# Optimization experiments

Hardware: AMD Instinct MI355X
Metric: run time of the kernel (lower is better)

## Reference

```python
import jax, jax.numpy as jnp
import numpy as np

N = 100000
E = 1600000
F_IN = 128
F_HID = 128


def gcn_conv(x, src, dst, deg_inv_sqrt, W, b, n_nodes):
    # x: [N, Fin] -> [N, Fout]; symmetric-normalized aggregation with self-loops
    h = x @ W  # [N, Fout]
    norm = deg_inv_sqrt[src] * deg_inv_sqrt[dst]  # [E+N] (self-loops appended)
    msgs = h[src] * norm[:, None]  # [E+N, Fout]
    out = jax.ops.segment_sum(msgs, dst, num_segments=n_nodes)
    return out + b


def setup_inputs() -> dict:
    key = jax.random.key(0)
    k = jax.random.split(key, 8)
    x = jax.random.normal(k[0], (N, F_IN), dtype=jnp.float32)
    edge_index = jax.random.randint(k[1], (2, E), 0, N, dtype=jnp.int32)
    s = 1.0 / np.sqrt(F_IN)
    W1 = jax.random.uniform(k[2], (F_IN, F_HID), jnp.float32, -s, s)
    b1 = jnp.zeros((F_HID,), jnp.float32)
    s2 = 1.0 / np.sqrt(F_HID)
    W2 = jax.random.uniform(k[3], (F_HID, F_HID), jnp.float32, -s2, s2)
    b2 = jnp.zeros((F_HID,), jnp.float32)
    W3 = jax.random.uniform(k[4], (F_HID, 1), jnp.float32, -s2, s2)
    b3 = jnp.zeros((1,), jnp.float32)
    return {"x": x, "edge_index": edge_index, "W1": W1, "b1": b1,
            "W2": W2, "b2": b2, "W3": W3, "b3": b3}


def reference(x, edge_index, W1, b1, W2, b2, W3, b3):
    n = x.shape[0]
    loops = jnp.arange(n, dtype=edge_index.dtype)
    src = jnp.concatenate([edge_index[0], loops])  # add self-loops
    dst = jnp.concatenate([edge_index[1], loops])
    deg = jax.ops.segment_sum(jnp.ones_like(dst, dtype=x.dtype), dst, num_segments=n)
    deg_inv_sqrt = jnp.where(deg > 0, jax.lax.rsqrt(deg), 0.0)

    h = gcn_conv(x, src, dst, deg_inv_sqrt, W1, b1, n)
    h = jax.nn.relu(h)  # dropout is identity at inference
    h = gcn_conv(h, src, dst, deg_inv_sqrt, W2, b2, n)
    h = jax.nn.relu(h)
    h = gcn_conv(h, src, dst, deg_inv_sqrt, W3, b3, n)
    return jax.nn.sigmoid(h)  # [N, 1]
```

## Files before the change

### kernel.cpp

```cpp
#include <hip/hip_runtime.h>
#include <cstdint>
#include <cstddef>

#define NN 100000
#define NE 1600000
#define FD 128
#define NXCD 8
#define RNODES ((NN + NXCD - 1) / NXCD)

typedef int vi4 __attribute__((ext_vector_type(4)));

__device__ __forceinline__ float bf_lo(uint32_t u) { return __uint_as_float(u << 16); }
__device__ __forceinline__ float bf_hi(uint32_t u) { return __uint_as_float(u & 0xffff0000u); }
__device__ __forceinline__ uint32_t bf_pack(float a, float b) {
    uint32_t ua = __float_as_uint(a), ub = __float_as_uint(b);
    ua += 0x7fffu + ((ua >> 16) & 1u);
    ub += 0x7fffu + ((ub >> 16) & 1u);
    return (ua >> 16) | (ub & 0xffff0000u);
}

__global__ __launch_bounds__(256) void k_hist(const int* __restrict__ dst,
                                              int* __restrict__ cnt, int e) {
    const int xcd   = blockIdx.x & 7;
    const int chunk = blockIdx.x >> 3;
    const int lo = xcd * RNODES;
    const int hi = lo + RNODES;
    const int base = chunk * 1024 + threadIdx.x * 4;
    if (base >= e) return;
    vi4 d4 = __builtin_nontemporal_load((const vi4*)(dst + base));
    #pragma unroll
    for (int j = 0; j < 4; ++j) {
        int d = d4[j];
        if (d >= lo && d < hi) atomicAdd(&cnt[d], 1);
    }
}

__global__ __launch_bounds__(1024) void k_scan1(const int* __restrict__ cnt,
                                                int* __restrict__ excl,
                                                int* __restrict__ bsum, int n) {
    __shared__ int sh[1024];
    int i = blockIdx.x * 1024 + threadIdx.x;
    int v = (i < n) ? cnt[i] : 0;
    sh[threadIdx.x] = v;
    __syncthreads();
    for (int off = 1; off < 1024; off <<= 1) {
        int t = (threadIdx.x >= off) ? sh[threadIdx.x - off] : 0;
        __syncthreads();
        sh[threadIdx.x] += t;
        __syncthreads();
    }
    if (i < n) excl[i] = sh[threadIdx.x] - v;
    if (threadIdx.x == 1023) bsum[blockIdx.x] = sh[1023];
}

__global__ void k_scan2(int* __restrict__ bsum, int nb) {
    __shared__ int sh[128];
    int t = threadIdx.x;
    int v = (t < nb) ? bsum[t] : 0;
    sh[t] = v;
    __syncthreads();
    for (int off = 1; off < 128; off <<= 1) {
        int u = (t >= off) ? sh[t - off] : 0;
        __syncthreads();
        sh[t] += u;
        __syncthreads();
    }
    if (t < nb) bsum[t] = sh[t] - v;
}

__global__ void k_scan3(int* __restrict__ excl, const int* __restrict__ bsum,
                        int* __restrict__ cursor, const int* __restrict__ cnt,
                        float* __restrict__ dis, int n, int e) {
    int i = blockIdx.x * blockDim.x + threadIdx.x;
    if (i < n) {
        int v = excl[i] + bsum[i >> 10];
        excl[i] = v;
        cursor[i] = v;
        dis[i] = rsqrtf((float)(cnt[i] + 1));
    }
    if (i == 0) excl[n] = e;
}

__global__ __launch_bounds__(256) void k_fill(const int* __restrict__ src,
                                              const int* __restrict__ dst,
                                              int* __restrict__ cursor,
                                              uint2* __restrict__ colw,
                                              const float* __restrict__ dis, int e) {
    const int xcd   = blockIdx.x & 7;
    const int chunk = blockIdx.x >> 3;
    const int lo = xcd * RNODES;
    const int hi = lo + RNODES;
    const int base = chunk * 1024 + threadIdx.x * 4;
    if (base >= e) return;
    vi4 d4 = __builtin_nontemporal_load((const vi4*)(dst + base));
    vi4 s4 = __builtin_nontemporal_load((const vi4*)(src + base));
    #pragma unroll
    for (int j = 0; j < 4; ++j) {
        int d = d4[j];
        if (d >= lo && d < hi) {
            int s   = s4[j];
            int pos = atomicAdd(&cursor[d], 1);
            uint2 cw;
            cw.x = (uint32_t)s;
            cw.y = __float_as_uint(dis[s] * dis[d]);
            colw[pos] = cw;
        }
    }
}

template <typename TIN>
__global__ __launch_bounds__(256) void k_gemm(const TIN* __restrict__ X,
                                              const float* __restrict__ W,
                                              unsigned short* __restrict__ H, int n) {
    __shared__ float At[64][68];
    __shared__ float Ws[64][64];
    const int t  = threadIdx.x;
    const int tx = t & 15;
    const int ty = t >> 4;
    const int rb = blockIdx.x * 64;
    const int cb = blockIdx.y * 64;

    float acc[4][4] = {};

    for (int c = 0; c < 2; ++c) {
        #pragma unroll
        for (int r = 0; r < 4; ++r) {
            int f   = t + 256 * r;
            int row = f >> 4;
            int kc  = (f & 15) << 2;
            int grow = rb + row;
            float4 v = make_float4(0.f, 0.f, 0.f, 0.f);
            if (grow < n) {
                if constexpr (sizeof(TIN) == 4) {
                    v = *(const float4*)((const float*)X + (size_t)grow * FD + c * 64 + kc);
                } else {
                    uint2 p = *(const uint2*)((const unsigned short*)X + (size_t)grow * FD + c * 64 + kc);
                    v.x = bf_lo(p.x); v.y = bf_hi(p.x);
                    v.z = bf_lo(p.y); v.w = bf_hi(p.y);
                }
            }
            At[kc + 0][row] = v.x;
            At[kc + 1][row] = v.y;
            At[kc + 2][row] = v.z;
            At[kc + 3][row] = v.w;
            *(float4*)&Ws[row][kc] =
                *(const float4*)(W + (size_t)(c * 64 + row) * FD + cb + kc);
        }
        __syncthreads();
        #pragma unroll 8
        for (int k = 0; k < 64; ++k) {
            float4 a = *(const float4*)&At[k][ty * 4];
            float4 b = *(const float4*)&Ws[k][tx * 4];
            acc[0][0] = fmaf(a.x, b.x, acc[0][0]);
            acc[0][1] = fmaf(a.x, b.y, acc[0][1]);
            acc[0][2] = fmaf(a.x, b.z, acc[0][2]);
            acc[0][3] = fmaf(a.x, b.w, acc[0][3]);
            acc[1][0] = fmaf(a.y, b.x, acc[1][0]);
            acc[1][1] = fmaf(a.y, b.y, acc[1][1]);
            acc[1][2] = fmaf(a.y, b.z, acc[1][2]);
            acc[1][3] = fmaf(a.y, b.w, acc[1][3]);
            acc[2][0] = fmaf(a.z, b.x, acc[2][0]);
            acc[2][1] = fmaf(a.z, b.y, acc[2][1]);
            acc[2][2] = fmaf(a.z, b.z, acc[2][2]);
            acc[2][3] = fmaf(a.z, b.w, acc[2][3]);
            acc[3][0] = fmaf(a.w, b.x, acc[3][0]);
            acc[3][1] = fmaf(a.w, b.y, acc[3][1]);
            acc[3][2] = fmaf(a.w, b.z, acc[3][2]);
            acc[3][3] = fmaf(a.w, b.w, acc[3][3]);
        }
        __syncthreads();
    }

    #pragma unroll
    for (int i = 0; i < 4; ++i) {
        int grow = rb + ty * 4 + i;
        if (grow < n) {
            uint2 p;
            p.x = bf_pack(acc[i][0], acc[i][1]);
            p.y = bf_pack(acc[i][2], acc[i][3]);
            *(uint2*)(H + (size_t)grow * FD + cb + tx * 4) = p;
        }
    }
}

template <int MODE>
__global__ __launch_bounds__(256) void k_agg(const unsigned short* __restrict__ h,
                                             const float* __restrict__ dis,
                                             const int* __restrict__ rp,
                                             const uint2* __restrict__ colw,
                                             const float* __restrict__ bias,
                                             const float* __restrict__ W3,
                                             unsigned short* __restrict__ out,
                                             float* __restrict__ outf, int n) {
    const uint32_t* h32 = (const uint32_t*)h;
    int wid  = (int)((blockIdx.x * (size_t)blockDim.x + threadIdx.x) >> 6);
    int lane = threadIdx.x & 63;
    int w2 = __builtin_amdgcn_readfirstlane(wid);
    int i0 = 2 * w2;
    if (i0 >= n) return;
    int i1 = i0 + 1;
    const bool has1 = (i1 < n);

    const int e00 = rp[i0];
    const int e01 = rp[i0 + 1];
    const int e11 = has1 ? rp[i0 + 2] : e01;

    float di0 = dis[i0];
    float di1 = has1 ? dis[i1] : 0.f;
    float2 acc0, acc1;
    {
        uint32_t su0 = h32[(size_t)i0 * 64 + lane];
        float q0 = di0 * di0;
        acc0.x = bf_lo(su0) * q0; acc0.y = bf_hi(su0) * q0;
        if (has1) {
            uint32_t su1 = h32[(size_t)i1 * 64 + lane];
            float q1 = di1 * di1;
            acc1.x = bf_lo(su1) * q1; acc1.y = bf_hi(su1) * q1;
        } else { acc1.x = acc1.y = 0.f; }
    }

    const int ng0 = (e01 - e00 + 15) >> 4;
    const int ng1 = (e11 - e01 + 15) >> 4;
    const int ng  = ng0 > ng1 ? ng0 : ng1;

    for (int g = 0; g < ng; ++g) {
        const bool do0 = (g < ng0), do1 = (g < ng1);
        int s0[16], s1[16];
        float w0_[16], w1_[16];
        uint32_t v0[16], v1[16];
        if (do0) {
            const int jb = e00 + g * 16;
            if (jb + 16 <= e01) {
                #pragma unroll
                for (int q = 0; q < 16; ++q) {
                    uint2 cw = colw[jb + q];
                    s0[q] = (int)cw.x; w0_[q] = __uint_as_float(cw.y);
                }
            } else {
                #pragma unroll
                for (int q = 0; q < 16; ++q) {
                    int idx = jb + q;
                    int c   = idx < e01 ? idx : e01 - 1;
                    uint2 cw = colw[c];
                    s0[q]  = (int)cw.x;
                    w0_[q] = idx < e01 ? __uint_as_float(cw.y) : 0.f;
                }
            }
        }
        if (do1) {
            const int jb = e01 + g * 16;
            if (jb + 16 <= e11) {
                #pragma unroll
                for (int q = 0; q < 16; ++q) {
                    uint2 cw = colw[jb + q];
                    s1[q] = (int)cw.x; w1_[q] = __uint_as_float(cw.y);
                }
            } else {
                #pragma unroll
                for (int q = 0; q < 16; ++q) {
                    int idx = jb + q;
                    int c   = idx < e11 ? idx : e11 - 1;
                    uint2 cw = colw[c];
                    s1[q]  = (int)cw.x;
                    w1_[q] = idx < e11 ? __uint_as_float(cw.y) : 0.f;
                }
            }
        }
        if (do0) {
            #pragma unroll
            for (int q = 0; q < 16; ++q)
                v0[q] = h32[(size_t)s0[q] * 64 + lane];
        }
        if (do1) {
            #pragma unroll
            for (int q = 0; q < 16; ++q)
                v1[q] = h32[(size_t)s1[q] * 64 + lane];
        }
        if (do0) {
            #pragma unroll
            for (int q = 0; q < 16; ++q) {
                acc0.x = fmaf(w0_[q], bf_lo(v0[q]), acc0.x);
                acc0.y = fmaf(w0_[q], bf_hi(v0[q]), acc0.y);
            }
        }
        if (do1) {
            #pragma unroll
            for (int q = 0; q < 16; ++q) {
                acc1.x = fmaf(w1_[q], bf_lo(v1[q]), acc1.x);
                acc1.y = fmaf(w1_[q], bf_hi(v1[q]), acc1.y);
            }
        }
    }

    float2 b = ((const float2*)bias)[lane];
    acc0.x = fmaxf(acc0.x + b.x, 0.f);
    acc0.y = fmaxf(acc0.y + b.y, 0.f);
    acc1.x = fmaxf(acc1.x + b.x, 0.f);
    acc1.y = fmaxf(acc1.y + b.y, 0.f);

    if (MODE == 0) {
        ((uint32_t*)out)[(size_t)i0 * 64 + lane] = bf_pack(acc0.x, acc0.y);
        if (has1)
            ((uint32_t*)out)[(size_t)i1 * 64 + lane] = bf_pack(acc1.x, acc1.y);
    } else {
        float2 w3 = ((const float2*)W3)[lane];
        float d0 = acc0.x * w3.x + acc0.y * w3.y;
        float d1 = acc1.x * w3.x + acc1.y * w3.y;
        #pragma unroll
        for (int off = 32; off; off >>= 1) {
            d0 += __shfl_xor(d0, off);
            d1 += __shfl_xor(d1, off);
        }
        if (lane == 0) {
            outf[i0] = d0;
            if (has1) outf[i1] = d1;
        }
    }
}

__global__ __launch_bounds__(256) void k_agg1(const float* __restrict__ h3,
                                              const float* __restrict__ dis,
                                              const int* __restrict__ rp,
                                              const uint2* __restrict__ colw,
                                              const float* __restrict__ b3,
                                              float* __restrict__ out, int n) {
    int i    = (int)((blockIdx.x * (size_t)blockDim.x + threadIdx.x) >> 6);
    int lane = threadIdx.x & 63;
    if (i >= n) return;
    float di  = dis[i];
    float acc = (lane == 0) ? di * di * h3[i] : 0.f;
    const int e0 = rp[i], e1 = rp[i + 1];
    for (int base = e0 + lane; base < e1; base += 64) {
        uint2 cw = colw[base];
        acc = fmaf(__uint_as_float(cw.y), h3[(int)cw.x], acc);
    }
    #pragma unroll
    for (int off = 32; off; off >>= 1) acc += __shfl_xor(acc, off);
    if (lane == 0) {
        float v = acc + b3[0];
        out[i] = 1.f / (1.f + expf(-v));
    }
}

static inline size_t alg(size_t x) { return (x + 255) & ~(size_t)255; }

extern "C" void kernel_launch(void* const* d_in, const int* in_sizes, int n_in,
                              void* d_out, int out_size, void* d_ws, size_t ws_size,
                              hipStream_t stream) {
    const float* x   = (const float*)d_in[0];
    const int*   ei  = (const int*)d_in[1];
    const float* W1  = (const float*)d_in[2];
    const float* b1  = (const float*)d_in[3];
    const float* W2  = (const float*)d_in[4];
    const float* b2  = (const float*)d_in[5];
    const float* W3  = (const float*)d_in[6];
    const float* b3  = (const float*)d_in[7];
    float*       out = (float*)d_out;

    const int n = NN, e = NE;
    const int* src = ei;
    const int* dst = ei + e;

    char* w = (char*)d_ws;
    float* dis    = (float*)w;  w += alg((size_t)n * 4);
    int*   cnt    = (int*)w;    w += alg((size_t)n * 4);
    int*   rp     = (int*)w;    w += alg((size_t)(n + 1) * 4);
    int*   cursor = (int*)w;    w += alg((size_t)n * 4);
    int*   bsum   = (int*)w;    w += alg((size_t)128 * 4);
    uint2* colw   = (uint2*)w;  w += alg((size_t)e * 8);
    unsigned short* bufA = (unsigned short*)w; w += alg((size_t)n * FD * 2);
    unsigned short* bufB = (unsigned short*)w; w += alg((size_t)n * FD * 2);
    float* h3     = (float*)w;  w += alg((size_t)n * 4);

    hipMemsetAsync(cnt, 0, (size_t)n * 4, stream);

    const int B = 256;
    const int gN = (n + B - 1) / B;
    const int nScan = (n + 1023) / 1024;
    const int nChunk = (e + 1023) / 1024;

    k_hist<<<nChunk * NXCD, B, 0, stream>>>(dst, cnt, e);
    k_scan1<<<nScan, 1024, 0, stream>>>(cnt, rp, bsum, n);
    k_scan2<<<1, 128, 0, stream>>>(bsum, nScan);
    k_scan3<<<gN, B, 0, stream>>>(rp, bsum, cursor, cnt, dis, n, e);
    k_fill<<<nChunk * NXCD, B, 0, stream>>>(src, dst, cursor, colw, dis, e);

    dim3 gGemm((n + 63) / 64, 2);
    const int nWave2  = (n + 1) / 2;
    const int gWave2  = (nWave2 * 64 + B - 1) / B;
    const int gWave   = (n * 64 + B - 1) / B;

    k_gemm<float><<<gGemm, B, 0, stream>>>(x, W1, bufA, n);
    k_agg<0><<<gWave2, B, 0, stream>>>(bufA, dis, rp, colw, b1, W3, bufB, h3, n);
    k_gemm<unsigned short><<<gGemm, B, 0, stream>>>(bufB, W2, bufA, n);
    k_agg<1><<<gWave2, B, 0, stream>>>(bufA, dis, rp, colw, b2, W3, bufB, h3, n);
    k_agg1<<<gWave, B, 0, stream>>>(h3, dis, rp, colw, b3, out, n);
}
```

Before: 531.4 us.

## Pre-partition edges into per-XCD buckets before histogram and CSR fill

```diff
diff --git a/kernel.cpp b/kernel.cpp
--- a/kernel.cpp
+++ b/kernel.cpp
@@ -7,6 +7,7 @@
 #define FD 128
 #define NXCD 8
 #define RNODES ((NN + NXCD - 1) / NXCD)
+#define CAP 208192
 
 typedef int vi4 __attribute__((ext_vector_type(4)));
 
@@ -19,20 +20,53 @@
     return (ua >> 16) | (ub & 0xffff0000u);
 }
 
-__global__ __launch_bounds__(256) void k_hist(const int* __restrict__ dst,
-                                              int* __restrict__ cnt, int e) {
-    const int xcd   = blockIdx.x & 7;
-    const int chunk = blockIdx.x >> 3;
+__global__ __launch_bounds__(256) void k_part(const int* __restrict__ src,
+                                              const int* __restrict__ dst,
+                                              uint32_t* __restrict__ bkt,
+                                              int* __restrict__ bcnt, int e) {
+    __shared__ int scnt[8];
+    __shared__ int sbase[8];
+    if (threadIdx.x < 8) scnt[threadIdx.x] = 0;
+    __syncthreads();
+    const int base = blockIdx.x * 1024 + threadIdx.x * 4;
+    const bool valid = base < e;
+    int b_[4]; int r_[4]; uint32_t u_[4];
+    if (valid) {
+        vi4 d4 = __builtin_nontemporal_load((const vi4*)(dst + base));
+        vi4 s4 = __builtin_nontemporal_load((const vi4*)(src + base));
+        #pragma unroll
+        for (int j = 0; j < 4; ++j) {
+            int d = d4[j], s = s4[j];
+            int b = d / RNODES;
+            b_[j] = b;
+            u_[j] = ((uint32_t)(d - b * RNODES) << 17) | (uint32_t)s;
+            r_[j] = atomicAdd(&scnt[b], 1);
+        }
+    }
+    __syncthreads();
+    if (threadIdx.x < 8)
+        sbase[threadIdx.x] = atomicAdd(&bcnt[threadIdx.x], scnt[threadIdx.x]);
+    __syncthreads();
+    if (valid) {
+        #pragma unroll
+        for (int j = 0; j < 4; ++j) {
+            int b = b_[j];
+            bkt[(size_t)b * CAP + sbase[b] + r_[j]] = u_[j];
+        }
+    }
+}
+
+__global__ __launch_bounds__(256) void k_hist2(const uint32_t* __restrict__ bkt,
+                                               const int* __restrict__ bcnt,
+                                               int* __restrict__ cnt) {
+    const int xcd  = blockIdx.x & 7;
+    const int blk  = blockIdx.x >> 3;
+    const int nblk = (int)(gridDim.x >> 3);
+    const int m = bcnt[xcd];
+    const uint32_t* B = bkt + (size_t)xcd * CAP;
     const int lo = xcd * RNODES;
-    const int hi = lo + RNODES;
-    const int base = chunk * 1024 + threadIdx.x * 4;
-    if (base >= e) return;
-    vi4 d4 = __builtin_nontemporal_load((const vi4*)(dst + base));
-    #pragma unroll
-    for (int j = 0; j < 4; ++j) {
-        int d = d4[j];
-        if (d >= lo && d < hi) atomicAdd(&cnt[d], 1);
-    }
+    for (int i = blk * 256 + threadIdx.x; i < m; i += nblk * 256)
+        atomicAdd(&cnt[lo + (int)(B[i] >> 17)], 1);
 }
 
 __global__ __launch_bounds__(1024) void k_scan1(const int* __restrict__ cnt,
@@ -81,30 +115,26 @@
     if (i == 0) excl[n] = e;
 }
 
-__global__ __launch_bounds__(256) void k_fill(const int* __restrict__ src,
-                                              const int* __restrict__ dst,
-                                              int* __restrict__ cursor,
-                                              uint2* __restrict__ colw,
-                                              const float* __restrict__ dis, int e) {
-    const int xcd   = blockIdx.x & 7;
-    const int chunk = blockIdx.x >> 3;
+__global__ __launch_bounds__(256) void k_fill2(const uint32_t* __restrict__ bkt,
+                                               const int* __restrict__ bcnt,
+                                               int* __restrict__ cursor,
+                                               uint2* __restrict__ colw,
+                                               const float* __restrict__ dis) {
+    const int xcd  = blockIdx.x & 7;
+    const int blk  = blockIdx.x >> 3;
+    const int nblk = (int)(gridDim.x >> 3);
+    const int m = bcnt[xcd];
+    const uint32_t* B = bkt + (size_t)xcd * CAP;
     const int lo = xcd * RNODES;
-    const int hi = lo + RNODES;
-    const int base = chunk * 1024 + threadIdx.x * 4;
-    if (base >= e) return;
-    vi4 d4 = __builtin_nontemporal_load((const vi4*)(dst + base));
-    vi4 s4 = __builtin_nontemporal_load((const vi4*)(src + base));
-    #pragma unroll
-    for (int j = 0; j < 4; ++j) {
-        int d = d4[j];
-        if (d >= lo && d < hi) {
-            int s   = s4[j];
-            int pos = atomicAdd(&cursor[d], 1);
-            uint2 cw;
-            cw.x = (uint32_t)s;
-            cw.y = __float_as_uint(dis[s] * dis[d]);
-            colw[pos] = cw;
-        }
+    for (int i = blk * 256 + threadIdx.x; i < m; i += nblk * 256) {
+        uint32_t u = B[i];
+        int s = (int)(u & 0x1FFFFu);
+        int d = lo + (int)(u >> 17);
+        int pos = atomicAdd(&cursor[d], 1);
+        uint2 cw;
+        cw.x = (uint32_t)s;
+        cw.y = __float_as_uint(dis[s] * dis[d]);
+        colw[pos] = cw;
     }
 }
 
@@ -364,26 +394,30 @@
     char* w = (char*)d_ws;
     float* dis    = (float*)w;  w += alg((size_t)n * 4);
     int*   cnt    = (int*)w;    w += alg((size_t)n * 4);
+    int*   bcnt   = (int*)w;    w += alg((size_t)8 * 4);
     int*   rp     = (int*)w;    w += alg((size_t)(n + 1) * 4);
     int*   cursor = (int*)w;    w += alg((size_t)n * 4);
     int*   bsum   = (int*)w;    w += alg((size_t)128 * 4);
+    uint32_t* bkt = (uint32_t*)w; w += alg((size_t)NXCD * CAP * 4);
     uint2* colw   = (uint2*)w;  w += alg((size_t)e * 8);
     unsigned short* bufA = (unsigned short*)w; w += alg((size_t)n * FD * 2);
     unsigned short* bufB = (unsigned short*)w; w += alg((size_t)n * FD * 2);
     float* h3     = (float*)w;  w += alg((size_t)n * 4);
 
     hipMemsetAsync(cnt, 0, (size_t)n * 4, stream);
+    hipMemsetAsync(bcnt, 0, 8 * 4, stream);
 
     const int B = 256;
     const int gN = (n + B - 1) / B;
     const int nScan = (n + 1023) / 1024;
     const int nChunk = (e + 1023) / 1024;
 
-    k_hist<<<nChunk * NXCD, B, 0, stream>>>(dst, cnt, e);
+    k_part<<<nChunk, B, 0, stream>>>(src, dst, bkt, bcnt, e);
+    k_hist2<<<2048, B, 0, stream>>>(bkt, bcnt, cnt);
     k_scan1<<<nScan, 1024, 0, stream>>>(cnt, rp, bsum, n);
     k_scan2<<<1, 128, 0, stream>>>(bsum, nScan);
     k_scan3<<<gN, B, 0, stream>>>(rp, bsum, cursor, cnt, dis, n, e);
-    k_fill<<<nChunk * NXCD, B, 0, stream>>>(src, dst, cursor, colw, dis, e);
+    k_fill2<<<2048, B, 0, stream>>>(bkt, bcnt, cursor, colw, dis);
 
     dim3 gGemm((n + 63) / 64, 2);
     const int nWave2  = (n + 1) / 2;
```

Result: no change. 525.1 us (-1.2%).
